# Performance work log

Measured on AMD Instinct MI355X. Metric: run time of the kernel, lower is better.

## Reference

```python
import jax, jax.numpy as jnp
import numpy as np

B, S, D, H = 4, 2048, 1024, 16
HD = D // H  # head dim = 64


def setup_inputs() -> dict:
    key = jax.random.key(0)
    ks = jax.random.split(key, 11)
    scale = 1.0 / np.sqrt(D)
    return {
        "q": jax.random.normal(ks[0], (B, S, D), jnp.float32),
        "k": jax.random.normal(ks[1], (B, S, D), jnp.float32),
        "v": jax.random.normal(ks[2], (B, S, D), jnp.float32),
        "w_q": jax.random.normal(ks[3], (D, D), jnp.float32) * scale,
        "b_q": jax.random.normal(ks[4], (D,), jnp.float32) * scale,
        "w_k": jax.random.normal(ks[5], (D, D), jnp.float32) * scale,
        "b_k": jax.random.normal(ks[6], (D,), jnp.float32) * scale,
        "w_v": jax.random.normal(ks[7], (D, D), jnp.float32) * scale,
        "b_v": jax.random.normal(ks[8], (D,), jnp.float32) * scale,
        "w_o": jax.random.normal(ks[9], (D, D), jnp.float32) * scale,
        "b_o": jax.random.normal(ks[10], (D,), jnp.float32) * scale,
    }


def _split_heads(x):
    # [B,S,D] -> [B,H,S,HD]
    return x.reshape(B, S, H, HD).transpose(0, 2, 1, 3)


def reference(q, k, v, w_q, b_q, w_k, b_k, w_v, b_v, w_o, b_o):
    qh = _split_heads(q @ w_q + b_q)
    kh = _split_heads(k @ w_k + b_k)
    vh = _split_heads(v @ w_v + b_v)
    # full score matrix [B,H,S,S], as in the naive torch code
    score = jnp.einsum("bhqd,bhkd->bhqk", qh, kh) / jnp.sqrt(jnp.float32(HD))
    attn = jax.nn.softmax(score, axis=-1)
    out = jnp.einsum("bhqk,bhkd->bhqd", attn, vh)
    out = out.transpose(0, 2, 1, 3).reshape(B, S, D)
    return out @ w_o + b_o
```

## Files before the change

### kernel.cpp

```cpp
#include <hip/hip_runtime.h>
#include <hip/hip_bf16.h>

#define BB 4
#define SS 2048
#define DD 1024
#define HH 16
#define HDD 64
#define MM (BB*SS)

using bf16x8 = __attribute__((ext_vector_type(8))) short;
using f32x4  = __attribute__((ext_vector_type(4))) float;
using f32x16 = __attribute__((ext_vector_type(16))) float;

static __device__ __forceinline__ ushort f2bf(float f) {
    __hip_bfloat16 h = __float2bfloat16(f);
    return *reinterpret_cast<ushort*>(&h);
}

static __device__ __forceinline__ void gload_lds16(const ushort* g, ushort* l) {
    __builtin_amdgcn_global_load_lds(
        (const __attribute__((address_space(1))) unsigned int*)g,
        (__attribute__((address_space(3))) unsigned int*)l, 16, 0, 0);
}

static __device__ __forceinline__ unsigned cvtpk(float lo, float hi) {
    unsigned r;
    asm("v_cvt_pk_bf16_f32 %0, %1, %2" : "=v"(r) : "v"(lo), "v"(hi));
    return r;
}

static __device__ __forceinline__ float exp2_raw(float x) {
    float r;
    asm("v_exp_f32 %0, %1" : "=v"(r) : "v"(x));
    return r;
}

static __device__ __forceinline__ void halfswap(unsigned& a, unsigned& b, int hi) {
#if __has_builtin(__builtin_amdgcn_permlane32_swap)
    typedef int v2i __attribute__((ext_vector_type(2)));
    v2i r = __builtin_amdgcn_permlane32_swap((int)a, (int)b, false, false);
    a = (unsigned)r.x; b = (unsigned)r.y;
#else
    unsigned xa = (unsigned)__shfl_xor((int)a, 32);
    unsigned xb = (unsigned)__shfl_xor((int)b, 32);
    unsigned na = hi ? xb : a;
    unsigned nb = hi ? b : xa;
    a = na; b = nb;
#endif
}

__global__ __launch_bounds__(256) void cast_bf16_k(
    const float* __restrict__ in, ushort* __restrict__ out)
{
    const size_t i = ((size_t)blockIdx.x * 256 + threadIdx.x) * 8;
    float4 a = *(const float4*)(in + i);
    float4 b = *(const float4*)(in + i + 4);
    short v[8];
    v[0] = (short)f2bf(a.x); v[1] = (short)f2bf(a.y);
    v[2] = (short)f2bf(a.z); v[3] = (short)f2bf(a.w);
    v[4] = (short)f2bf(b.x); v[5] = (short)f2bf(b.y);
    v[6] = (short)f2bf(b.z); v[7] = (short)f2bf(b.w);
    *(bf16x8*)(out + i) = *(const bf16x8*)v;
}

__global__ __launch_bounds__(256) void wtrans_k(
    const float* __restrict__ w0, const float* __restrict__ w1,
    const float* __restrict__ w2, const float* __restrict__ w3,
    ushort* __restrict__ o0, ushort* __restrict__ o1,
    ushort* __restrict__ o2, ushort* __restrict__ o3)
{
    __shared__ float tile[32][33];
    const float* W; ushort* O;
    switch (blockIdx.z) {
        case 0:  W = w0; O = o0; break;
        case 1:  W = w1; O = o1; break;
        case 2:  W = w2; O = o2; break;
        default: W = w3; O = o3; break;
    }
    const int tx = threadIdx.x & 31, ty = threadIdx.x >> 5;
    const int n0 = blockIdx.x * 32, k0 = blockIdx.y * 32;
    #pragma unroll
    for (int i = 0; i < 4; i++)
        tile[ty * 4 + i][tx] = W[(size_t)(k0 + ty * 4 + i) * DD + n0 + tx];
    __syncthreads();
    #pragma unroll
    for (int i = 0; i < 4; i++)
        O[(size_t)(n0 + ty * 4 + i) * DD + k0 + tx] = f2bf(tile[tx][ty * 4 + i]);
}

template<int MODE>
__global__ __launch_bounds__(256) void gemm_mfma_k(
    const ushort* __restrict__ A, const ushort* __restrict__ WT,
    const float* __restrict__ bias, void* __restrict__ Cout)
{
    __shared__ ushort As[128 * 32];
    __shared__ ushort Bs[128 * 32];

    const int t  = threadIdx.x;
    const int w  = t >> 6;
    const int l  = t & 63;
    const int lr = l & 15;
    const int lg = l >> 4;
    const int wr = w >> 1, wc = w & 1;

    int bid = blockIdx.x;
    bid = (bid & 7) * 64 + (bid >> 3);
    const int mt = bid >> 3, nt = bid & 7;
    const int m0 = mt * 128, n0 = nt * 128;

    const int srow = l >> 2;
    const int scol = (l & 3) * 8;

    f32x4 acc[4][4];
    #pragma unroll
    for (int mi = 0; mi < 4; mi++)
        #pragma unroll
        for (int ni = 0; ni < 4; ni++)
            acc[mi][ni] = (f32x4){0.f, 0.f, 0.f, 0.f};

    const ushort* Ab = A  + (size_t)m0 * DD;
    const ushort* Bb = WT + (size_t)n0 * DD;

    for (int k0 = 0; k0 < DD; k0 += 32) {
        __syncthreads();
        #pragma unroll
        for (int j = 0; j < 2; j++) {
            const int rbase = (w * 2 + j) * 16;
            gload_lds16(Ab + (size_t)(rbase + srow) * DD + k0 + scol, &As[rbase * 32]);
            gload_lds16(Bb + (size_t)(rbase + srow) * DD + k0 + scol, &Bs[rbase * 32]);
        }
        __syncthreads();

        bf16x8 af[4], bfr[4];
        #pragma unroll
        for (int mi = 0; mi < 4; mi++)
            af[mi] = *(const bf16x8*)&As[(wr * 64 + mi * 16 + lr) * 32 + lg * 8];
        #pragma unroll
        for (int ni = 0; ni < 4; ni++)
            bfr[ni] = *(const bf16x8*)&Bs[(wc * 64 + ni * 16 + lr) * 32 + lg * 8];
        #pragma unroll
        for (int mi = 0; mi < 4; mi++)
            #pragma unroll
            for (int ni = 0; ni < 4; ni++)
                acc[mi][ni] = __builtin_amdgcn_mfma_f32_16x16x32_bf16(
                    af[mi], bfr[ni], acc[mi][ni], 0, 0, 0);
    }

    #pragma unroll
    for (int mi = 0; mi < 4; mi++) {
        #pragma unroll
        for (int ni = 0; ni < 4; ni++) {
            const int c  = n0 + wc * 64 + ni * 16 + lr;
            const float bc = bias[c];
            const int r0 = m0 + wr * 64 + mi * 16 + lg * 4;
            if (MODE == 0) {
                float* Co = (float*)Cout;
                #pragma unroll
                for (int rg = 0; rg < 4; rg++)
                    Co[(size_t)(r0 + rg) * DD + c] = acc[mi][ni][rg] + bc;
            } else if (MODE == 3) {
                const int bi = r0 >> 11, si = r0 & 2047;
                const int hi = c >> 6,  hd = c & 63;
                ushort pk[4];
                #pragma unroll
                for (int rg = 0; rg < 4; rg++)
                    pk[rg] = f2bf(acc[mi][ni][rg] + bc);
                ushort* O = (ushort*)Cout;
                *(uint2*)&O[(((size_t)(bi * HH + hi) * HDD) + hd) * SS + si] =
                    *(const uint2*)pk;
            } else {
                const float sc = (MODE == 2) ? 0.180336880111f : 1.0f;
                ushort* O = (ushort*)Cout;
                #pragma unroll
                for (int rg = 0; rg < 4; rg++) {
                    const int r = r0 + rg;
                    const int bi = r >> 11, si = r & 2047;
                    const int hi = c >> 6,  hd = c & 63;
                    O[(((size_t)(bi * HH + hi) * SS) + si) * HDD + hd] =
                        f2bf((acc[mi][ni][rg] + bc) * sc);
                }
            }
        }
    }
}

__global__ __launch_bounds__(256) void flash_attn_mfma(
    const ushort* __restrict__ qh, const ushort* __restrict__ kh,
    const ushort* __restrict__ vt, ushort* __restrict__ ctx)
{
    __shared__ ushort smem[20480];

    const int t  = threadIdx.x;
    const int w  = t >> 6;
    const int l  = t & 63;
    const int hi = l >> 5;
    const int lq = l & 31;

    const int q0 = blockIdx.x * 128;
    const int h  = blockIdx.y;
    const int bi = blockIdx.z;
    const size_t base  = (size_t)(bi * HH + h) * SS * HDD;
    const size_t basev = (size_t)(bi * HH + h) * HDD * SS;

    bf16x8 qf[4];
    {
        const ushort* qp = qh + base + (size_t)(q0 + w * 32 + lq) * HDD;
        #pragma unroll
        for (int ds = 0; ds < 4; ds++)
            qf[ds] = *(const bf16x8*)(qp + ds * 16 + hi * 8);
    }

    f32x16 o0 = {}, o1 = {};
    float l_loc = 0.f;

    const int rsub = l >> 3;
    const int csw  = ((l & 7) ^ rsub) * 8;
    auto stageK = [&](int buf, int kv) {
        #pragma unroll
        for (int j = 0; j < 2; j++) {
            const int rb = 16 * w + 8 * j;
            gload_lds16(kh + base + (size_t)(kv + rb + rsub) * HDD + csw,
                        &smem[buf * 4096 + rb * 64]);
        }
    };
    auto stageV = [&](int buf, int kv) {
        #pragma unroll
        for (int j = 0; j < 2; j++) {
            const int rb = 16 * w + 8 * j;
            gload_lds16(vt + basev + (size_t)(rb + rsub) * SS + kv + csw,
                        &smem[8192 + buf * 4096 + rb * 64]);
        }
    };

    auto qk = [&](int kbuf, f32x16& s0, f32x16& s1) {
        const ushort* KB = &smem[kbuf * 4096];
        s0 = (f32x16){};
        s1 = (f32x16){};
        __builtin_amdgcn_s_setprio(1);
        #pragma unroll
        for (int ds = 0; ds < 4; ds++) {
            const int slot = ((ds * 2 + hi) ^ (l & 7)) * 8;
            bf16x8 ka0 = *(const bf16x8*)&KB[lq * 64 + slot];
            bf16x8 ka1 = *(const bf16x8*)&KB[(32 + lq) * 64 + slot];
            s0 = __builtin_amdgcn_mfma_f32_32x32x16_bf16(ka0, qf[ds], s0, 0, 0, 0);
            s1 = __builtin_amdgcn_mfma_f32_32x32x16_bf16(ka1, qf[ds], s1, 0, 0, 0);
        }
        __builtin_amdgcn_s_setprio(0);
    };

    auto finish = [&](f32x16& s0, f32x16& s1, bf16x8* pa) {
        float t0 = 0.f, t1 = 0.f, t2 = 0.f, t3 = 0.f;
        #pragma unroll
        for (int r = 0; r < 16; r += 4) {
            s0[r + 0] = exp2_raw(s0[r + 0]); t0 += s0[r + 0];
            s0[r + 1] = exp2_raw(s0[r + 1]); t1 += s0[r + 1];
            s0[r + 2] = exp2_raw(s0[r + 2]); t2 += s0[r + 2];
            s0[r + 3] = exp2_raw(s0[r + 3]); t3 += s0[r + 3];
        }
        #pragma unroll
        for (int r = 0; r < 16; r += 4) {
            s1[r + 0] = exp2_raw(s1[r + 0]); t0 += s1[r + 0];
            s1[r + 1] = exp2_raw(s1[r + 1]); t1 += s1[r + 1];
            s1[r + 2] = exp2_raw(s1[r + 2]); t2 += s1[r + 2];
            s1[r + 3] = exp2_raw(s1[r + 3]); t3 += s1[r + 3];
        }
        l_loc += (t0 + t1) + (t2 + t3);
        #pragma unroll
        for (int sblk = 0; sblk < 4; sblk++) {
            const int ob = (sblk & 1) * 8;
            float e0, e1, e2, e3, e4, e5, e6, e7;
            if (sblk < 2) {
                e0 = s0[ob + 0]; e1 = s0[ob + 1]; e2 = s0[ob + 2]; e3 = s0[ob + 3];
                e4 = s0[ob + 4]; e5 = s0[ob + 5]; e6 = s0[ob + 6]; e7 = s0[ob + 7];
            } else {
                e0 = s1[ob + 0]; e1 = s1[ob + 1]; e2 = s1[ob + 2]; e3 = s1[ob + 3];
                e4 = s1[ob + 4]; e5 = s1[ob + 5]; e6 = s1[ob + 6]; e7 = s1[ob + 7];
            }
            unsigned a = cvtpk(e0, e1);
            unsigned b = cvtpk(e4, e5);
            halfswap(a, b, hi);
            unsigned c = cvtpk(e2, e3);
            unsigned d = cvtpk(e6, e7);
            halfswap(c, d, hi);
            union { unsigned u[4]; bf16x8 v; } fr;
            fr.u[0] = a; fr.u[1] = c; fr.u[2] = b; fr.u[3] = d;
            pa[sblk] = fr.v;
        }
    };

    auto pv = [&](int vbuf, const bf16x8* pa) {
        const ushort* VB = &smem[8192 + vbuf * 4096];
        __builtin_amdgcn_s_setprio(1);
        #pragma unroll
        for (int ks = 0; ks < 4; ks++) {
            const int slot = ((ks * 2 + hi) ^ (l & 7)) * 8;
            bf16x8 vb0 = *(const bf16x8*)&VB[lq * 64 + slot];
            bf16x8 vb1 = *(const bf16x8*)&VB[(32 + lq) * 64 + slot];
            o0 = __builtin_amdgcn_mfma_f32_32x32x16_bf16(pa[ks], vb0, o0, 0, 0, 0);
            o1 = __builtin_amdgcn_mfma_f32_32x32x16_bf16(pa[ks], vb1, o1, 0, 0, 0);
        }
        __builtin_amdgcn_s_setprio(0);
    };

    stageK(0, 0);  stageV(0, 0);
    __syncthreads();
    stageK(1, 64); stageV(1, 64);
    f32x16 sA0, sA1, sB0, sB1;
    qk(0, sA0, sA1);

    int vA = 0, vB = 1, vS = 2;
    bf16x8 pa[4];

    for (int tt = 0; tt < 32; tt += 2) {
        __syncthreads();
        if (tt + 2 < 32) { stageK(0, (tt + 2) * 64); stageV(vS, (tt + 2) * 64); }
        qk(1, sB0, sB1);
        finish(sA0, sA1, pa);
        pv(vA, pa);

        __syncthreads();
        if (tt + 3 < 32) { stageK(1, (tt + 3) * 64); stageV(vA, (tt + 3) * 64); }
        if (tt + 2 < 32) qk(0, sA0, sA1);
        finish(sB0, sB1, pa);
        pv(vB, pa);

        const int tmp = vS;
        vS = vB; vB = vA; vA = tmp;
    }

    const float l_sum = l_loc + __shfl_xor(l_loc, 32);
    const float invl  = 1.0f / l_sum;
    #pragma unroll
    for (int r = 0; r < 16; r++) {
        const int qq = (r & 3) + 8 * (r >> 2) + 4 * hi;
        const float iv = __shfl(invl, qq);
        const int row = q0 + w * 32 + qq;
        ushort* op = ctx + (size_t)(bi * SS + row) * DD + h * HDD;
        op[lq]      = f2bf(o0[r] * iv);
        op[32 + lq] = f2bf(o1[r] * iv);
    }
}

extern "C" void kernel_launch(void* const* d_in, const int* in_sizes, int n_in,
                              void* d_out, int out_size, void* d_ws, size_t ws_size,
                              hipStream_t stream) {
    const float* q   = (const float*)d_in[0];
    const float* k   = (const float*)d_in[1];
    const float* v   = (const float*)d_in[2];
    const float* w_q = (const float*)d_in[3];
    const float* b_q = (const float*)d_in[4];
    const float* w_k = (const float*)d_in[5];
    const float* b_k = (const float*)d_in[6];
    const float* w_v = (const float*)d_in[7];
    const float* b_v = (const float*)d_in[8];
    const float* w_o = (const float*)d_in[9];
    const float* b_o = (const float*)d_in[10];
    float* out = (float*)d_out;

    const size_t SZ = (size_t)BB * SS * DD;
    const size_t WZ = (size_t)DD * DD;
    ushort* ws2  = (ushort*)d_ws;
    ushort* qh   = ws2;
    ushort* kh   = ws2 + SZ;
    ushort* vt   = ws2 + 2 * SZ;
    ushort* ctxb = ws2 + 3 * SZ;
    ushort* qbf  = ws2 + 4 * SZ;
    ushort* kbf  = ws2 + 5 * SZ;
    ushort* vbf  = ws2 + 6 * SZ;
    ushort* wqT  = ws2 + 7 * SZ;
    ushort* wkT  = wqT + WZ;
    ushort* wvT  = wkT + WZ;
    ushort* woT  = wvT + WZ;

    const int castBlocks = (int)(SZ / (256 * 8));
    cast_bf16_k<<<castBlocks, 256, 0, stream>>>(q, qbf);
    cast_bf16_k<<<castBlocks, 256, 0, stream>>>(k, kbf);
    cast_bf16_k<<<castBlocks, 256, 0, stream>>>(v, vbf);
    wtrans_k<<<dim3(32, 32, 4), 256, 0, stream>>>(w_q, w_k, w_v, w_o,
                                                  wqT, wkT, wvT, woT);

    const int gblocks = (MM / 128) * (DD / 128);
    gemm_mfma_k<2><<<gblocks, 256, 0, stream>>>(qbf, wqT, b_q, qh);
    gemm_mfma_k<1><<<gblocks, 256, 0, stream>>>(kbf, wkT, b_k, kh);
    gemm_mfma_k<3><<<gblocks, 256, 0, stream>>>(vbf, wvT, b_v, vt);

    flash_attn_mfma<<<dim3(SS / 128, HH, BB), 256, 0, stream>>>(qh, kh, vt, ctxb);

    gemm_mfma_k<0><<<gblocks, 256, 0, stream>>>(ctxb, woT, b_o, out);
}
```

Baseline: 225.9 us.

## Triple-buffer K/V in flash attention with vmcnt barriers, XCD-aware grid, fused cast

The attention kernel now triple-buffers K as well as V and replaces __syncthreads with explicit vmcnt waits plus raw s_barrier. This lets loads for later tiles stay in flight across the barrier, and V is staged one iteration later. The grid is flattened to 1D and remapped so that consecutive blocks of the same head land on the same XCD, which should improve L2 reuse of K/V. The three input cast kernels are merged into one launch. The cost is more LDS per block, which may lower occupancy, and a fragile hand-counted vmcnt scheme.

```diff
diff --git a/kernel.cpp b/kernel.cpp
--- a/kernel.cpp
+++ b/kernel.cpp
@@ -49,18 +49,33 @@
 #endif
 }
 
-__global__ __launch_bounds__(256) void cast_bf16_k(
-    const float* __restrict__ in, ushort* __restrict__ out)
+#define PIPE_BAR(N) do {                                          \
+    asm volatile("s_waitcnt vmcnt(" #N ")" ::: "memory");         \
+    __builtin_amdgcn_sched_barrier(0);                            \
+    __builtin_amdgcn_s_barrier();                                 \
+    __builtin_amdgcn_sched_barrier(0);                            \
+} while (0)
+
+__global__ __launch_bounds__(256) void cast3_bf16_k(
+    const float* __restrict__ q, const float* __restrict__ k,
+    const float* __restrict__ v, ushort* __restrict__ qo,
+    ushort* __restrict__ ko, ushort* __restrict__ vo)
 {
+    const float* in; ushort* out;
+    switch (blockIdx.y) {
+        case 0:  in = q; out = qo; break;
+        case 1:  in = k; out = ko; break;
+        default: in = v; out = vo; break;
+    }
     const size_t i = ((size_t)blockIdx.x * 256 + threadIdx.x) * 8;
     float4 a = *(const float4*)(in + i);
     float4 b = *(const float4*)(in + i + 4);
-    short v[8];
-    v[0] = (short)f2bf(a.x); v[1] = (short)f2bf(a.y);
-    v[2] = (short)f2bf(a.z); v[3] = (short)f2bf(a.w);
-    v[4] = (short)f2bf(b.x); v[5] = (short)f2bf(b.y);
-    v[6] = (short)f2bf(b.z); v[7] = (short)f2bf(b.w);
-    *(bf16x8*)(out + i) = *(const bf16x8*)v;
+    short r[8];
+    r[0] = (short)f2bf(a.x); r[1] = (short)f2bf(a.y);
+    r[2] = (short)f2bf(a.z); r[3] = (short)f2bf(a.w);
+    r[4] = (short)f2bf(b.x); r[5] = (short)f2bf(b.y);
+    r[6] = (short)f2bf(b.z); r[7] = (short)f2bf(b.w);
+    *(bf16x8*)(out + i) = *(const bf16x8*)r;
 }
 
 __global__ __launch_bounds__(256) void wtrans_k(
@@ -188,7 +203,7 @@
     const ushort* __restrict__ qh, const ushort* __restrict__ kh,
     const ushort* __restrict__ vt, ushort* __restrict__ ctx)
 {
-    __shared__ ushort smem[20480];
+    __shared__ ushort smem[24576];
 
     const int t  = threadIdx.x;
     const int w  = t >> 6;
@@ -196,9 +211,11 @@
     const int hi = l >> 5;
     const int lq = l & 31;
 
-    const int q0 = blockIdx.x * 128;
-    const int h  = blockIdx.y;
-    const int bi = blockIdx.z;
+    const int wg = (blockIdx.x & 7) * 128 + (blockIdx.x >> 3);
+    const int bi = wg >> 8;
+    const int h  = (wg >> 4) & 15;
+    const int q0 = (wg & 15) * 128;
+
     const size_t base  = (size_t)(bi * HH + h) * SS * HDD;
     const size_t basev = (size_t)(bi * HH + h) * HDD * SS;
 
@@ -228,7 +245,7 @@
         for (int j = 0; j < 2; j++) {
             const int rb = 16 * w + 8 * j;
             gload_lds16(vt + basev + (size_t)(rb + rsub) * SS + kv + csw,
-                        &smem[8192 + buf * 4096 + rb * 64]);
+                        &smem[12288 + buf * 4096 + rb * 64]);
         }
     };
 
@@ -289,7 +306,7 @@
     };
 
     auto pv = [&](int vbuf, const bf16x8* pa) {
-        const ushort* VB = &smem[8192 + vbuf * 4096];
+        const ushort* VB = &smem[12288 + vbuf * 4096];
         __builtin_amdgcn_s_setprio(1);
         #pragma unroll
         for (int ks = 0; ks < 4; ks++) {
@@ -302,31 +319,43 @@
         __builtin_amdgcn_s_setprio(0);
     };
 
-    stageK(0, 0);  stageV(0, 0);
-    __syncthreads();
-    stageK(1, 64); stageV(1, 64);
     f32x16 sA0, sA1, sB0, sB1;
+    bf16x8 pa[4];
+    stageK(0, 0); stageK(1, 64); stageV(0, 0);
+    PIPE_BAR(4);
     qk(0, sA0, sA1);
 
-    int vA = 0, vB = 1, vS = 2;
-    bf16x8 pa[4];
-
-    for (int tt = 0; tt < 32; tt += 2) {
-        __syncthreads();
-        if (tt + 2 < 32) { stageK(0, (tt + 2) * 64); stageV(vS, (tt + 2) * 64); }
-        qk(1, sB0, sB1);
+    int ka = 1, kb = 2, kc = 0;
+    int va = 0, vb = 1, vc = 2;
+
+    for (int tt = 0; tt < 30; tt += 2) {
+        stageK(kb, (tt + 2) * 64);
+        PIPE_BAR(2);
+        stageV(vb, (tt + 1) * 64);
+        qk(ka, sB0, sB1);
         finish(sA0, sA1, pa);
-        pv(vA, pa);
-
-        __syncthreads();
-        if (tt + 3 < 32) { stageK(1, (tt + 3) * 64); stageV(vA, (tt + 3) * 64); }
-        if (tt + 2 < 32) qk(0, sA0, sA1);
+        pv(va, pa);
+        { int k2 = ka; ka = kb; kb = kc; kc = k2;
+          int v2 = va; va = vb; vb = vc; vc = v2; }
+
+        stageK(kb, (tt + 3) * 64);
+        PIPE_BAR(2);
+        stageV(vb, (tt + 2) * 64);
+        qk(ka, sA0, sA1);
         finish(sB0, sB1, pa);
-        pv(vB, pa);
-
-        const int tmp = vS;
-        vS = vB; vB = vA; vA = tmp;
-    }
+        pv(va, pa);
+        { int k2 = ka; ka = kb; kb = kc; kc = k2;
+          int v2 = va; va = vb; vb = vc; vc = v2; }
+    }
+
+    PIPE_BAR(0);
+    stageV(vb, 31 * 64);
+    qk(ka, sB0, sB1);
+    finish(sA0, sA1, pa);
+    pv(va, pa);
+    PIPE_BAR(0);
+    finish(sB0, sB1, pa);
+    pv(vb, pa);
 
     const float l_sum = l_loc + __shfl_xor(l_loc, 32);
     const float invl  = 1.0f / l_sum;
@@ -373,9 +402,7 @@
     ushort* woT  = wvT + WZ;
 
     const int castBlocks = (int)(SZ / (256 * 8));
-    cast_bf16_k<<<castBlocks, 256, 0, stream>>>(q, qbf);
-    cast_bf16_k<<<castBlocks, 256, 0, stream>>>(k, kbf);
-    cast_bf16_k<<<castBlocks, 256, 0, stream>>>(v, vbf);
+    cast3_bf16_k<<<dim3(castBlocks, 3), 256, 0, stream>>>(q, k, v, qbf, kbf, vbf);
     wtrans_k<<<dim3(32, 32, 4), 256, 0, stream>>>(w_q, w_k, w_v, w_o,
                                                   wqT, wkT, wvT, woT);
 
@@ -384,7 +411,7 @@
     gemm_mfma_k<1><<<gblocks, 256, 0, stream>>>(kbf, wkT, b_k, kh);
     gemm_mfma_k<3><<<gblocks, 256, 0, stream>>>(vbf, wvT, b_v, vt);
 
-    flash_attn_mfma<<<dim3(SS / 128, HH, BB), 256, 0, stream>>>(qh, kh, vt, ctxb);
+    flash_attn_mfma<<<dim3(1024), 256, 0, stream>>>(qh, kh, vt, ctxb);
 
     gemm_mfma_k<0><<<gblocks, 256, 0, stream>>>(ctxb, woT, b_o, out);
 }
```

New measurement: 220.7 us. 2.3% less time.
